# Kernel optimization log

Measured on AMD Instinct MI355X. Metric: run time of the kernel, lower is better.

## Reference

```python
import jax, jax.numpy as jnp
import numpy as np

N_NODES = 100000
N_EDGES = 1600000
IN_CH = 128
HID = 64
OUT_CH = 16
N_GRAPHS = 512
NEG_SLOPE = 0.2


def setup_inputs() -> dict:
    key = jax.random.key(0)
    ks = jax.random.split(key, 24)
    x = jax.random.normal(ks[0], (N_NODES, IN_CH), dtype=jnp.float32)
    edge_index = jax.random.randint(ks[1], (2, N_EDGES), 0, N_NODES, dtype=jnp.int64)
    batch = jnp.sort(jax.random.randint(ks[2], (N_NODES,), 0, N_GRAPHS, dtype=jnp.int64))
    s = 0.05
    p = {
        'W_l1': jax.random.normal(ks[3], (IN_CH, HID)) * s,
        'b_l1': jnp.zeros((HID,), jnp.float32),
        'W_r1': jax.random.normal(ks[4], (IN_CH, HID)) * s,
        'b_r1': jnp.zeros((HID,), jnp.float32),
        'att1': jax.random.normal(ks[5], (HID,)) * s,
        'bias1': jnp.zeros((HID,), jnp.float32),
        'W_l2': jax.random.normal(ks[6], (HID, HID)) * s,
        'b_l2': jnp.zeros((HID,), jnp.float32),
        'W_r2': jax.random.normal(ks[7], (HID, HID)) * s,
        'b_r2': jnp.zeros((HID,), jnp.float32),
        'att2': jax.random.normal(ks[8], (HID,)) * s,
        'bias2': jnp.zeros((HID,), jnp.float32),
        'W_fc1': jax.random.normal(ks[9], (HID, HID)) * s,
        'b_fc1': jnp.zeros((HID,), jnp.float32),
        'gamma': jnp.ones((HID,), jnp.float32),
        'beta': jnp.zeros((HID,), jnp.float32),
        'W_fc2': jax.random.normal(ks[10], (HID, OUT_CH)) * s,
        'b_fc2': jnp.zeros((OUT_CH,), jnp.float32),
    }
    return dict(x=x, edge_index=edge_index, batch=batch, **p)


def _gatv2_layer(x, src, dst, Wl, bl, Wr, br, att, bias):
    # GATv2Conv (heads=1): x_l = lin_l(x), x_r = lin_r(x)
    xl = x @ Wl + bl              # [N, H] source transform
    xr = x @ Wr + br              # [N, H] target transform
    # per-edge score: att . LeakyReLU(x_l[j] + x_r[i])
    h = xl[src] + xr[dst]         # [E, H]
    h = jnp.where(h >= 0, h, NEG_SLOPE * h)
    e = h @ att                   # [E]
    # scatter-softmax over incoming edges of each target node
    m = jax.ops.segment_max(e, dst, num_segments=N_NODES)
    a = jnp.exp(e - m[dst])
    z = jax.ops.segment_sum(a, dst, num_segments=N_NODES)
    alpha = a / z[dst]            # every node has a self-loop -> z > 0
    out = jax.ops.segment_sum(alpha[:, None] * xl[src], dst, num_segments=N_NODES)
    return out + bias


def reference(x, edge_index, batch, W_l1, b_l1, W_r1, b_r1, att1, bias1,
              W_l2, b_l2, W_r2, b_r2, att2, bias2,
              W_fc1, b_fc1, gamma, beta, W_fc2, b_fc2):
    loop = jnp.arange(N_NODES, dtype=edge_index.dtype)
    src = jnp.concatenate([edge_index[0], loop])  # add_self_loops=True
    dst = jnp.concatenate([edge_index[1], loop])
    h = _gatv2_layer(x, src, dst, W_l1, b_l1, W_r1, b_r1, att1, bias1)
    h = jax.nn.relu(h)
    h = _gatv2_layer(h, src, dst, W_l2, b_l2, W_r2, b_r2, att2, bias2)
    # global mean pool over graphs
    sums = jax.ops.segment_sum(h, batch, num_segments=N_GRAPHS)
    cnt = jax.ops.segment_sum(jnp.ones((N_NODES,), h.dtype), batch, num_segments=N_GRAPHS)
    g = sums / jnp.clip(cnt, 1.0)[:, None]        # [G, H]
    # MLP head: Linear -> BatchNorm1d (training-mode batch stats) -> ReLU -> Linear
    y = g @ W_fc1 + b_fc1
    mu = jnp.mean(y, axis=0)
    var = jnp.var(y, axis=0)
    y = gamma * (y - mu) * jax.lax.rsqrt(var + 1e-5) + beta
    y = jax.nn.relu(y)
    y = y @ W_fc2 + b_fc2
    return jax.nn.log_softmax(y, axis=1)
```

## Files before the change

kernel.cpp:

```cpp
#include <hip/hip_runtime.h>

#define N_NODES 100000
#define N_EDGES 1600000
#define IN_CH 128
#define HID 64
#define OUT_CH 16
#define N_GRAPHS 512
#define NEG_SLOPE 0.2f

#define MAX_DEG 64

#define GEMM1_BLOCKS ((N_NODES + 127) / 128)
#define DEG_EPT 8
#define DEG_BLOCKS ((N_EDGES + 256 * DEG_EPT - 1) / (256 * DEG_EPT))
#define FUSED_BLOCKS (GEMM1_BLOCKS + DEG_BLOCKS)

#define NEG_BIG (-1e30f)
#define LDSP 132

__device__ __forceinline__ unsigned int f2bf_pack(float lo, float hi) {
  unsigned int ul = __float_as_uint(lo);
  unsigned int uh = __float_as_uint(hi);
  ul = (ul + 0x7FFFu + ((ul >> 16) & 1u)) >> 16;
  uh = (uh + 0x7FFFu + ((uh >> 16) & 1u)) >> 16;
  return ul | (uh << 16);
}
__device__ __forceinline__ float bf2f(unsigned short b) {
  return __uint_as_float(((unsigned int)b) << 16);
}


__global__ __launch_bounds__(256) void k_fused_gemm1_scatter(
    const float* __restrict__ x,
    const float* __restrict__ Wl, const float* __restrict__ bl,
    const float* __restrict__ Wr, const float* __restrict__ br,
    unsigned short* __restrict__ xlb, unsigned short* __restrict__ xrb,
    const int* __restrict__ src, const int* __restrict__ dst,
    int* __restrict__ deg, int* __restrict__ adjP) {
  constexpr int K = IN_CH;
  constexpr int KC = 16;
  constexpr int NCH = K / KC;
  __shared__ float xs[KC][LDSP];
  __shared__ float ws[KC][LDSP];

  int b = blockIdx.x;
  if (b & 1) {
    int db = b >> 1;
    int base = (db * 256 + threadIdx.x) * DEG_EPT;
    if (base + DEG_EPT <= N_EDGES) {
      int4 d4a = *(const int4*)&dst[base];
      int4 d4b = *(const int4*)&dst[base + 4];
      int4 s4a = *(const int4*)&src[base];
      int4 s4b = *(const int4*)&src[base + 4];
      int sl;
      sl = atomicAdd(&deg[d4a.x], 1); if (sl < MAX_DEG) adjP[d4a.x * MAX_DEG + sl] = s4a.x;
      sl = atomicAdd(&deg[d4a.y], 1); if (sl < MAX_DEG) adjP[d4a.y * MAX_DEG + sl] = s4a.y;
      sl = atomicAdd(&deg[d4a.z], 1); if (sl < MAX_DEG) adjP[d4a.z * MAX_DEG + sl] = s4a.z;
      sl = atomicAdd(&deg[d4a.w], 1); if (sl < MAX_DEG) adjP[d4a.w * MAX_DEG + sl] = s4a.w;
      sl = atomicAdd(&deg[d4b.x], 1); if (sl < MAX_DEG) adjP[d4b.x * MAX_DEG + sl] = s4b.x;
      sl = atomicAdd(&deg[d4b.y], 1); if (sl < MAX_DEG) adjP[d4b.y * MAX_DEG + sl] = s4b.y;
      sl = atomicAdd(&deg[d4b.z], 1); if (sl < MAX_DEG) adjP[d4b.z * MAX_DEG + sl] = s4b.z;
      sl = atomicAdd(&deg[d4b.w], 1); if (sl < MAX_DEG) adjP[d4b.w * MAX_DEG + sl] = s4b.w;
    } else {
      for (int e = base; e < N_EDGES; e++) {
        int d = dst[e];
        int sl = atomicAdd(&deg[d], 1);
        if (sl < MAX_DEG) adjP[d * MAX_DEG + sl] = src[e];
      }
    }
    return;
  }

  int tid = threadIdx.x;
  int tx = tid & 15;
  int ty = tid >> 4;
  int nb = (b >> 1) * 128;

  float acc[8][8];
  #pragma unroll
  for (int i = 0; i < 8; i++)
    #pragma unroll
    for (int j = 0; j < 8; j++) acc[i][j] = 0.f;

  for (int c = 0; c < NCH; c++) {
    int kc = c * KC;
    if (c) __syncthreads();
    #pragma unroll
    for (int j = 0; j < 2; j++) {
      int idx = tid + 256 * j;
      int node = idx >> 2, q = idx & 3;
      int gn = nb + node;
      float4 v = make_float4(0.f, 0.f, 0.f, 0.f);
      if (gn < N_NODES) v = *(const float4*)&x[(size_t)gn * K + kc + q * 4];
      xs[q * 4 + 0][node] = v.x;
      xs[q * 4 + 1][node] = v.y;
      xs[q * 4 + 2][node] = v.z;
      xs[q * 4 + 3][node] = v.w;
    }
    #pragma unroll
    for (int j = 0; j < 2; j++) {
      int idx = tid + 256 * j;
      int k = idx >> 5, cc = idx & 31;
      float4 v;
      if (cc < 16) v = *(const float4*)&Wl[(size_t)(kc + k) * 64 + cc * 4];
      else         v = *(const float4*)&Wr[(size_t)(kc + k) * 64 + (cc - 16) * 4];
      *(float4*)&ws[k][cc * 4] = v;
    }
    __syncthreads();

    #pragma unroll 4
    for (int k = 0; k < KC; k++) {
      float4 a0 = *(const float4*)&xs[k][ty * 8];
      float4 a1 = *(const float4*)&xs[k][ty * 8 + 4];
      float4 b0 = *(const float4*)&ws[k][tx * 8];
      float4 b1 = *(const float4*)&ws[k][tx * 8 + 4];
      float av[8] = {a0.x, a0.y, a0.z, a0.w, a1.x, a1.y, a1.z, a1.w};
      float bv[8] = {b0.x, b0.y, b0.z, b0.w, b1.x, b1.y, b1.z, b1.w};
      #pragma unroll
      for (int i = 0; i < 8; i++)
        #pragma unroll
        for (int j = 0; j < 8; j++)
          acc[i][j] = fmaf(av[i], bv[j], acc[i][j]);
    }
  }

  int f0 = tx * 8;
  float bb[8];
  #pragma unroll
  for (int j = 0; j < 8; j++)
    bb[j] = (f0 < 64) ? bl[f0 + j] : br[f0 - 64 + j];
  unsigned short* outp = (f0 < 64) ? xlb : xrb;
  int fo = (f0 < 64) ? f0 : f0 - 64;
  #pragma unroll
  for (int i = 0; i < 8; i++) {
    int node = nb + ty * 8 + i;
    if (node < N_NODES) {
      int4 o;
      o.x = (int)f2bf_pack(acc[i][0] + bb[0], acc[i][1] + bb[1]);
      o.y = (int)f2bf_pack(acc[i][2] + bb[2], acc[i][3] + bb[3]);
      o.z = (int)f2bf_pack(acc[i][4] + bb[4], acc[i][5] + bb[5]);
      o.w = (int)f2bf_pack(acc[i][6] + bb[6], acc[i][7] + bb[7]);
      *(int4*)&outp[(size_t)node * 64 + fo] = o;
    }
  }
}


template <int K>
__global__ __launch_bounds__(256) void k_dual_gemm(
    const float* __restrict__ x,
    const float* __restrict__ Wl, const float* __restrict__ bl,
    const float* __restrict__ Wr, const float* __restrict__ br,
    unsigned short* __restrict__ xlb, unsigned short* __restrict__ xrb) {
  constexpr int KC = 32;
  constexpr int NCH = K / KC;
  __shared__ float xs[KC][LDSP];
  __shared__ float ws[KC][LDSP];

  int tid = threadIdx.x;
  int tx = tid & 15;
  int ty = tid >> 4;
  int nb = blockIdx.x * 128;

  float acc[8][8];
  #pragma unroll
  for (int i = 0; i < 8; i++)
    #pragma unroll
    for (int j = 0; j < 8; j++) acc[i][j] = 0.f;

  for (int c = 0; c < NCH; c++) {
    int kc = c * KC;
    if (c) __syncthreads();
    #pragma unroll
    for (int j = 0; j < 4; j++) {
      int idx = tid + 256 * j;
      int node = idx >> 3, q = idx & 7;
      int gn = nb + node;
      float4 v = make_float4(0.f, 0.f, 0.f, 0.f);
      if (gn < N_NODES) v = *(const float4*)&x[(size_t)gn * K + kc + q * 4];
      xs[q * 4 + 0][node] = v.x;
      xs[q * 4 + 1][node] = v.y;
      xs[q * 4 + 2][node] = v.z;
      xs[q * 4 + 3][node] = v.w;
    }
    #pragma unroll
    for (int j = 0; j < 4; j++) {
      int idx = tid + 256 * j;
      int k = idx >> 5, cc = idx & 31;
      float4 v;
      if (cc < 16) v = *(const float4*)&Wl[(size_t)(kc + k) * 64 + cc * 4];
      else         v = *(const float4*)&Wr[(size_t)(kc + k) * 64 + (cc - 16) * 4];
      *(float4*)&ws[k][cc * 4] = v;
    }
    __syncthreads();

    #pragma unroll 4
    for (int k = 0; k < KC; k++) {
      float4 a0 = *(const float4*)&xs[k][ty * 8];
      float4 a1 = *(const float4*)&xs[k][ty * 8 + 4];
      float4 b0 = *(const float4*)&ws[k][tx * 8];
      float4 b1 = *(const float4*)&ws[k][tx * 8 + 4];
      float av[8] = {a0.x, a0.y, a0.z, a0.w, a1.x, a1.y, a1.z, a1.w};
      float bv[8] = {b0.x, b0.y, b0.z, b0.w, b1.x, b1.y, b1.z, b1.w};
      #pragma unroll
      for (int i = 0; i < 8; i++)
        #pragma unroll
        for (int j = 0; j < 8; j++)
          acc[i][j] = fmaf(av[i], bv[j], acc[i][j]);
    }
  }

  int f0 = tx * 8;
  float bb[8];
  #pragma unroll
  for (int j = 0; j < 8; j++)
    bb[j] = (f0 < 64) ? bl[f0 + j] : br[f0 - 64 + j];
  unsigned short* outp = (f0 < 64) ? xlb : xrb;
  int fo = (f0 < 64) ? f0 : f0 - 64;
  #pragma unroll
  for (int i = 0; i < 8; i++) {
    int node = nb + ty * 8 + i;
    if (node < N_NODES) {
      int4 o;
      o.x = (int)f2bf_pack(acc[i][0] + bb[0], acc[i][1] + bb[1]);
      o.y = (int)f2bf_pack(acc[i][2] + bb[2], acc[i][3] + bb[3]);
      o.z = (int)f2bf_pack(acc[i][4] + bb[4], acc[i][5] + bb[5]);
      o.w = (int)f2bf_pack(acc[i][6] + bb[6], acc[i][7] + bb[7]);
      *(int4*)&outp[(size_t)node * 64 + fo] = o;
    }
  }
}


__global__ __launch_bounds__(256) void k_gat(
    const unsigned short* __restrict__ xlb, const unsigned short* __restrict__ xrb,
    const float* __restrict__ att, const float* __restrict__ bias,
    const int* __restrict__ deg, const int* __restrict__ adjP,
    float* __restrict__ out, int do_relu) {
  int wid = (blockIdx.x * 256 + threadIdx.x) >> 6;
  int lane = threadIdx.x & 63;
  if (wid >= N_NODES) return;
  int fg = lane & 15;
  int sub = lane >> 4;

  int degv = deg[wid];
  degv = (degv < MAX_DEG) ? degv : MAX_DEG;
  int L = degv + 1;

  int eidx = wid;
  if (lane < degv) eidx = adjP[(size_t)wid * MAX_DEG + lane];

  ushort4 xrr = *(const ushort4*)&xrb[(size_t)wid * 64 + fg * 4];
  float4 xr4;
  xr4.x = bf2f(xrr.x); xr4.y = bf2f(xrr.y); xr4.z = bf2f(xrr.z); xr4.w = bf2f(xrr.w);
  float4 att4 = *(const float4*)&att[fg * 4];

  float m = NEG_BIG, z = 0.f;
  float4 acc = make_float4(0.f, 0.f, 0.f, 0.f);

  for (int p0 = 0; p0 < L; p0 += 8) {
    int q0 = p0 + sub * 2;
    int q1 = q0 + 1;
    bool act0 = (q0 < L);
    bool act1 = (q1 < L);
    int idx0 = q0 - 1;
    int idx1 = q1 - 1;
    int sj0 = __shfl(eidx, idx0 & 63, 64);
    int sj1 = __shfl(eidx, idx1 & 63, 64);
    int j0 = (q0 == 0) ? wid : sj0;
    int j1 = sj1;
    ushort4 raw0 = make_ushort4(0, 0, 0, 0);
    ushort4 raw1 = make_ushort4(0, 0, 0, 0);
    if (act0) raw0 = *(const ushort4*)&xlb[(size_t)j0 * 64 + fg * 4];
    if (act1) raw1 = *(const ushort4*)&xlb[(size_t)j1 * 64 + fg * 4];
    float4 v0, v1;
    v0.x = bf2f(raw0.x); v0.y = bf2f(raw0.y); v0.z = bf2f(raw0.z); v0.w = bf2f(raw0.w);
    v1.x = bf2f(raw1.x); v1.y = bf2f(raw1.y); v1.z = bf2f(raw1.z); v1.w = bf2f(raw1.w);

    float ax, ay, az, aw;
    ax = v0.x + xr4.x; ax = (ax >= 0.f) ? ax : NEG_SLOPE * ax;
    ay = v0.y + xr4.y; ay = (ay >= 0.f) ? ay : NEG_SLOPE * ay;
    az = v0.z + xr4.z; az = (az >= 0.f) ? az : NEG_SLOPE * az;
    aw = v0.w + xr4.w; aw = (aw >= 0.f) ? aw : NEG_SLOPE * aw;
    float s0 = fmaf(ax, att4.x, fmaf(ay, att4.y, fmaf(az, att4.z, aw * att4.w)));
    ax = v1.x + xr4.x; ax = (ax >= 0.f) ? ax : NEG_SLOPE * ax;
    ay = v1.y + xr4.y; ay = (ay >= 0.f) ? ay : NEG_SLOPE * ay;
    az = v1.z + xr4.z; az = (az >= 0.f) ? az : NEG_SLOPE * az;
    aw = v1.w + xr4.w; aw = (aw >= 0.f) ? aw : NEG_SLOPE * aw;
    float s1 = fmaf(ax, att4.x, fmaf(ay, att4.y, fmaf(az, att4.z, aw * att4.w)));
    #pragma unroll
    for (int o = 1; o <= 8; o <<= 1) {
      s0 += __shfl_xor(s0, o, 64);
      s1 += __shfl_xor(s1, o, 64);
    }
    float e0 = act0 ? s0 : NEG_BIG;
    float e1 = act1 ? s1 : NEG_BIG;

    float nm = fmaxf(m, fmaxf(e0, e1));
    float sc = __expf(m - nm);
    float w0 = __expf(e0 - nm);
    float w1 = __expf(e1 - nm);
    z = fmaf(z, sc, w0 + w1);
    acc.x = fmaf(acc.x, sc, fmaf(w0, v0.x, w1 * v1.x));
    acc.y = fmaf(acc.y, sc, fmaf(w0, v0.y, w1 * v1.y));
    acc.z = fmaf(acc.z, sc, fmaf(w0, v0.z, w1 * v1.z));
    acc.w = fmaf(acc.w, sc, fmaf(w0, v0.w, w1 * v1.w));
    m = nm;
  }

  #pragma unroll
  for (int o = 16; o <= 32; o <<= 1) {
    float m2 = __shfl_xor(m, o, 64);
    float z2 = __shfl_xor(z, o, 64);
    float a0 = __shfl_xor(acc.x, o, 64);
    float a1 = __shfl_xor(acc.y, o, 64);
    float a2 = __shfl_xor(acc.z, o, 64);
    float a3 = __shfl_xor(acc.w, o, 64);
    float nm = fmaxf(m, m2);
    float s1 = __expf(m - nm);
    float s2 = __expf(m2 - nm);
    z = z * s1 + z2 * s2;
    acc.x = acc.x * s1 + a0 * s2;
    acc.y = acc.y * s1 + a1 * s2;
    acc.z = acc.z * s1 + a2 * s2;
    acc.w = acc.w * s1 + a3 * s2;
    m = nm;
  }

  if (sub == 0) {
    float4 b4 = *(const float4*)&bias[fg * 4];
    float inv = 1.f / z;
    float4 r;
    r.x = acc.x * inv + b4.x;
    r.y = acc.y * inv + b4.y;
    r.z = acc.z * inv + b4.z;
    r.w = acc.w * inv + b4.w;
    if (do_relu) {
      r.x = fmaxf(r.x, 0.f); r.y = fmaxf(r.y, 0.f);
      r.z = fmaxf(r.z, 0.f); r.w = fmaxf(r.w, 0.f);
    }
    *(float4*)&out[(size_t)wid * 64 + fg * 4] = r;
  }
}


__device__ __forceinline__ int lower_bound_batch(const int* __restrict__ b, int key) {
  int lo = 0, hi = N_NODES;
  while (lo < hi) {
    int mid = (lo + hi) >> 1;
    if (b[mid] < key) lo = mid + 1; else hi = mid;
  }
  return lo;
}

__global__ void k_pool(const float* __restrict__ h, const int* __restrict__ batch,
                       float* __restrict__ gmean) {
  __shared__ int s_range[2];
  __shared__ float red[256];
  int g = blockIdx.x, t = threadIdx.x;
  if (t == 0) s_range[0] = lower_bound_batch(batch, g);
  if (t == 1) s_range[1] = lower_bound_batch(batch, g + 1);
  __syncthreads();
  int lo = s_range[0], hi = s_range[1];
  int f = t & 63, sub = t >> 6;
  float acc = 0.f;
  for (int n = lo + sub; n < hi; n += 4) acc += h[n * 64 + f];
  red[t] = acc;
  __syncthreads();
  if (sub == 0) {
    float s = red[f] + red[64 + f] + red[128 + f] + red[192 + f];
    int cnt = hi - lo;
    if (cnt < 1) cnt = 1;
    gmean[g * 64 + f] = s / (float)cnt;
  }
}


__global__ void k_head1(const float* __restrict__ gmean, const float* __restrict__ W,
                        const float* __restrict__ b, float* __restrict__ y) {
  int idx = blockIdx.x * 256 + threadIdx.x;
  if (idx >= N_GRAPHS * 64) return;
  int gi = idx >> 6, f = idx & 63;
  float acc = b[f];
  #pragma unroll 8
  for (int k = 0; k < 64; k++) acc = fmaf(gmean[gi * 64 + k], W[k * 64 + f], acc);
  y[idx] = acc;
}

__global__ void k_bnstats(const float* __restrict__ y, float* __restrict__ mu,
                          float* __restrict__ rstd) {
  __shared__ float red_s[256], red_ss[256];
  int t = threadIdx.x;
  int f = t & 63, grp = t >> 6;
  float s = 0.f, ss = 0.f;
  for (int g = grp; g < N_GRAPHS; g += 4) {
    float v = y[g * 64 + f];
    s += v;
    ss += v * v;
  }
  red_s[t] = s;
  red_ss[t] = ss;
  __syncthreads();
  if (t < 64) {
    s = red_s[t] + red_s[64 + t] + red_s[128 + t] + red_s[192 + t];
    ss = red_ss[t] + red_ss[64 + t] + red_ss[128 + t] + red_ss[192 + t];
    float m = s / (float)N_GRAPHS;
    float var = ss / (float)N_GRAPHS - m * m;
    mu[t] = m;
    rstd[t] = rsqrtf(var + 1e-5f);
  }
}

__global__ void k_head2(const float* __restrict__ y, const float* __restrict__ gamma,
                        const float* __restrict__ beta, const float* __restrict__ mu,
                        const float* __restrict__ rstd, const float* __restrict__ W2,
                        const float* __restrict__ b2, float* __restrict__ out) {
  int idx = blockIdx.x * 256 + threadIdx.x;
  if (idx >= N_GRAPHS * OUT_CH) return;
  int gi = idx >> 4, o = idx & 15;
  float acc = b2[o];
  #pragma unroll
  for (int k = 0; k < 64; k++) {
    float v = y[gi * 64 + k];
    v = gamma[k] * (v - mu[k]) * rstd[k] + beta[k];
    v = fmaxf(v, 0.f);
    acc = fmaf(v, W2[k * OUT_CH + o], acc);
  }
  float mx = acc;
  #pragma unroll
  for (int w = 8; w > 0; w >>= 1) mx = fmaxf(mx, __shfl_xor(mx, w, 16));
  float ex = __expf(acc - mx);
  float s = ex;
  #pragma unroll
  for (int w = 8; w > 0; w >>= 1) s += __shfl_xor(s, w, 16);
  out[idx] = acc - mx - __logf(s);
}


extern "C" void kernel_launch(void* const* d_in, const int* in_sizes, int n_in,
                              void* d_out, int out_size, void* d_ws, size_t ws_size,
                              hipStream_t stream) {
  const float* x      = (const float*)d_in[0];
  const int*   edge   = (const int*)d_in[1];
  const int*   batch  = (const int*)d_in[2];
  const float* W_l1   = (const float*)d_in[3];
  const float* b_l1   = (const float*)d_in[4];
  const float* W_r1   = (const float*)d_in[5];
  const float* b_r1   = (const float*)d_in[6];
  const float* att1   = (const float*)d_in[7];
  const float* bias1  = (const float*)d_in[8];
  const float* W_l2   = (const float*)d_in[9];
  const float* b_l2   = (const float*)d_in[10];
  const float* W_r2   = (const float*)d_in[11];
  const float* b_r2   = (const float*)d_in[12];
  const float* att2   = (const float*)d_in[13];
  const float* bias2  = (const float*)d_in[14];
  const float* W_fc1  = (const float*)d_in[15];
  const float* b_fc1  = (const float*)d_in[16];
  const float* gamma  = (const float*)d_in[17];
  const float* beta   = (const float*)d_in[18];
  const float* W_fc2  = (const float*)d_in[19];
  const float* b_fc2  = (const float*)d_in[20];

  const int* src = edge;
  const int* dst = edge + N_EDGES;

  char* ws = (char*)d_ws;
  size_t off = 0;
  auto alloc = [&](size_t bytes) -> void* {
    off = (off + 255) & ~(size_t)255;
    void* p = ws + off;
    off += bytes;
    return p;
  };
  int* deg      = (int*)alloc((size_t)N_NODES * 4);
  int* adjP     = (int*)alloc((size_t)N_NODES * MAX_DEG * 4);
  unsigned short* xlb = (unsigned short*)alloc((size_t)N_NODES * HID * 2);
  unsigned short* xrb = (unsigned short*)alloc((size_t)N_NODES * HID * 2);
  float* h      = (float*)alloc((size_t)N_NODES * HID * 4);
  float* gmean  = (float*)alloc((size_t)N_GRAPHS * HID * 4);
  float* y      = (float*)alloc((size_t)N_GRAPHS * HID * 4);
  float* mu     = (float*)alloc(64 * 4);
  float* rstd   = (float*)alloc(64 * 4);

  hipMemsetAsync(deg, 0, (size_t)N_NODES * 4, stream);

  k_fused_gemm1_scatter<<<FUSED_BLOCKS, 256, 0, stream>>>(
      x, W_l1, b_l1, W_r1, b_r1, xlb, xrb, src, dst, deg, adjP);

  k_gat<<<(N_NODES + 3) / 4, 256, 0, stream>>>(xlb, xrb, att1, bias1, deg, adjP, h, 1);
  k_dual_gemm<HID><<<(N_NODES + 127) / 128, 256, 0, stream>>>(h, W_l2, b_l2, W_r2, b_r2, xlb, xrb);
  k_gat<<<(N_NODES + 3) / 4, 256, 0, stream>>>(xlb, xrb, att2, bias2, deg, adjP, h, 0);

  k_pool<<<N_GRAPHS, 256, 0, stream>>>(h, batch, gmean);
  k_head1<<<(N_GRAPHS * 64 + 255) / 256, 256, 0, stream>>>(gmean, W_fc1, b_fc1, y);
  k_bnstats<<<1, 256, 0, stream>>>(y, mu, rstd);
  k_head2<<<(N_GRAPHS * OUT_CH + 255) / 256, 256, 0, stream>>>(y, gamma, beta, mu, rstd,
                                                               W_fc2, b_fc2, (float*)d_out);
}
```

Baseline: 438.8 us.

## Partition edge scatter into destination-range buckets across 8 block groups

```diff
diff --git a/kernel.cpp b/kernel.cpp
--- a/kernel.cpp
+++ b/kernel.cpp
@@ -13,7 +13,9 @@
 #define GEMM1_BLOCKS ((N_NODES + 127) / 128)
 #define DEG_EPT 8
 #define DEG_BLOCKS ((N_EDGES + 256 * DEG_EPT - 1) / (256 * DEG_EPT))
-#define FUSED_BLOCKS (GEMM1_BLOCKS + DEG_BLOCKS)
+#define SCAT_BLOCKS (DEG_BLOCKS * 8)
+#define FUSED_BLOCKS (SCAT_BLOCKS + GEMM1_BLOCKS)
+#define NODES_PER_BUCKET (N_NODES / 8)
 
 #define NEG_BIG (-1e30f)
 #define LDSP 132
@@ -44,28 +46,33 @@
   __shared__ float ws[KC][LDSP];
 
   int b = blockIdx.x;
-  if (b & 1) {
-    int db = b >> 1;
-    int base = (db * 256 + threadIdx.x) * DEG_EPT;
+  if (b < SCAT_BLOCKS) {
+    int w = b >> 3;
+    int myb = b & 7;
+    int lo = myb * NODES_PER_BUCKET;
+    int hi = lo + NODES_PER_BUCKET;
+    int base = (w * 256 + threadIdx.x) * DEG_EPT;
     if (base + DEG_EPT <= N_EDGES) {
       int4 d4a = *(const int4*)&dst[base];
       int4 d4b = *(const int4*)&dst[base + 4];
       int4 s4a = *(const int4*)&src[base];
       int4 s4b = *(const int4*)&src[base + 4];
       int sl;
-      sl = atomicAdd(&deg[d4a.x], 1); if (sl < MAX_DEG) adjP[d4a.x * MAX_DEG + sl] = s4a.x;
-      sl = atomicAdd(&deg[d4a.y], 1); if (sl < MAX_DEG) adjP[d4a.y * MAX_DEG + sl] = s4a.y;
-      sl = atomicAdd(&deg[d4a.z], 1); if (sl < MAX_DEG) adjP[d4a.z * MAX_DEG + sl] = s4a.z;
-      sl = atomicAdd(&deg[d4a.w], 1); if (sl < MAX_DEG) adjP[d4a.w * MAX_DEG + sl] = s4a.w;
-      sl = atomicAdd(&deg[d4b.x], 1); if (sl < MAX_DEG) adjP[d4b.x * MAX_DEG + sl] = s4b.x;
-      sl = atomicAdd(&deg[d4b.y], 1); if (sl < MAX_DEG) adjP[d4b.y * MAX_DEG + sl] = s4b.y;
-      sl = atomicAdd(&deg[d4b.z], 1); if (sl < MAX_DEG) adjP[d4b.z * MAX_DEG + sl] = s4b.z;
-      sl = atomicAdd(&deg[d4b.w], 1); if (sl < MAX_DEG) adjP[d4b.w * MAX_DEG + sl] = s4b.w;
+      if (d4a.x >= lo && d4a.x < hi) { sl = atomicAdd(&deg[d4a.x], 1); if (sl < MAX_DEG) adjP[d4a.x * MAX_DEG + sl] = s4a.x; }
+      if (d4a.y >= lo && d4a.y < hi) { sl = atomicAdd(&deg[d4a.y], 1); if (sl < MAX_DEG) adjP[d4a.y * MAX_DEG + sl] = s4a.y; }
+      if (d4a.z >= lo && d4a.z < hi) { sl = atomicAdd(&deg[d4a.z], 1); if (sl < MAX_DEG) adjP[d4a.z * MAX_DEG + sl] = s4a.z; }
+      if (d4a.w >= lo && d4a.w < hi) { sl = atomicAdd(&deg[d4a.w], 1); if (sl < MAX_DEG) adjP[d4a.w * MAX_DEG + sl] = s4a.w; }
+      if (d4b.x >= lo && d4b.x < hi) { sl = atomicAdd(&deg[d4b.x], 1); if (sl < MAX_DEG) adjP[d4b.x * MAX_DEG + sl] = s4b.x; }
+      if (d4b.y >= lo && d4b.y < hi) { sl = atomicAdd(&deg[d4b.y], 1); if (sl < MAX_DEG) adjP[d4b.y * MAX_DEG + sl] = s4b.y; }
+      if (d4b.z >= lo && d4b.z < hi) { sl = atomicAdd(&deg[d4b.z], 1); if (sl < MAX_DEG) adjP[d4b.z * MAX_DEG + sl] = s4b.z; }
+      if (d4b.w >= lo && d4b.w < hi) { sl = atomicAdd(&deg[d4b.w], 1); if (sl < MAX_DEG) adjP[d4b.w * MAX_DEG + sl] = s4b.w; }
     } else {
       for (int e = base; e < N_EDGES; e++) {
         int d = dst[e];
-        int sl = atomicAdd(&deg[d], 1);
-        if (sl < MAX_DEG) adjP[d * MAX_DEG + sl] = src[e];
+        if (d >= lo && d < hi) {
+          int sl = atomicAdd(&deg[d], 1);
+          if (sl < MAX_DEG) adjP[d * MAX_DEG + sl] = src[e];
+        }
       }
     }
     return;
@@ -74,7 +81,7 @@
   int tid = threadIdx.x;
   int tx = tid & 15;
   int ty = tid >> 4;
-  int nb = (b >> 1) * 128;
+  int nb = (b - SCAT_BLOCKS) * 128;
 
   float acc[8][8];
   #pragma unroll
```

After: 462.2 us. 5.3% more time.

## Build adjacency via bucketed counting sort instead of global atomics

Applied to the files above, without the earlier changes.

```diff
diff --git a/kernel.cpp b/kernel.cpp
--- a/kernel.cpp
+++ b/kernel.cpp
@@ -10,10 +10,9 @@
 
 #define MAX_DEG 64
 
-#define GEMM1_BLOCKS ((N_NODES + 127) / 128)
-#define DEG_EPT 8
-#define DEG_BLOCKS ((N_EDGES + 256 * DEG_EPT - 1) / (256 * DEG_EPT))
-#define FUSED_BLOCKS (GEMM1_BLOCKS + DEG_BLOCKS)
+#define NBUCK ((N_NODES + 255) >> 8)
+#define NCB 128
+#define EDGE_WIN ((N_EDGES + NCB - 1) / NCB)
 
 #define NEG_BIG (-1e30f)
 #define LDSP 132
@@ -30,119 +29,91 @@
 }
 
 
-__global__ __launch_bounds__(256) void k_fused_gemm1_scatter(
-    const float* __restrict__ x,
-    const float* __restrict__ Wl, const float* __restrict__ bl,
-    const float* __restrict__ Wr, const float* __restrict__ br,
-    unsigned short* __restrict__ xlb, unsigned short* __restrict__ xrb,
-    const int* __restrict__ src, const int* __restrict__ dst,
-    int* __restrict__ deg, int* __restrict__ adjP) {
-  constexpr int K = IN_CH;
-  constexpr int KC = 16;
-  constexpr int NCH = K / KC;
-  __shared__ float xs[KC][LDSP];
-  __shared__ float ws[KC][LDSP];
-
-  int b = blockIdx.x;
-  if (b & 1) {
-    int db = b >> 1;
-    int base = (db * 256 + threadIdx.x) * DEG_EPT;
-    if (base + DEG_EPT <= N_EDGES) {
-      int4 d4a = *(const int4*)&dst[base];
-      int4 d4b = *(const int4*)&dst[base + 4];
-      int4 s4a = *(const int4*)&src[base];
-      int4 s4b = *(const int4*)&src[base + 4];
-      int sl;
-      sl = atomicAdd(&deg[d4a.x], 1); if (sl < MAX_DEG) adjP[d4a.x * MAX_DEG + sl] = s4a.x;
-      sl = atomicAdd(&deg[d4a.y], 1); if (sl < MAX_DEG) adjP[d4a.y * MAX_DEG + sl] = s4a.y;
-      sl = atomicAdd(&deg[d4a.z], 1); if (sl < MAX_DEG) adjP[d4a.z * MAX_DEG + sl] = s4a.z;
-      sl = atomicAdd(&deg[d4a.w], 1); if (sl < MAX_DEG) adjP[d4a.w * MAX_DEG + sl] = s4a.w;
-      sl = atomicAdd(&deg[d4b.x], 1); if (sl < MAX_DEG) adjP[d4b.x * MAX_DEG + sl] = s4b.x;
-      sl = atomicAdd(&deg[d4b.y], 1); if (sl < MAX_DEG) adjP[d4b.y * MAX_DEG + sl] = s4b.y;
-      sl = atomicAdd(&deg[d4b.z], 1); if (sl < MAX_DEG) adjP[d4b.z * MAX_DEG + sl] = s4b.z;
-      sl = atomicAdd(&deg[d4b.w], 1); if (sl < MAX_DEG) adjP[d4b.w * MAX_DEG + sl] = s4b.w;
-    } else {
-      for (int e = base; e < N_EDGES; e++) {
-        int d = dst[e];
-        int sl = atomicAdd(&deg[d], 1);
-        if (sl < MAX_DEG) adjP[d * MAX_DEG + sl] = src[e];
-      }
-    }
-    return;
-  }
-
-  int tid = threadIdx.x;
-  int tx = tid & 15;
-  int ty = tid >> 4;
-  int nb = (b >> 1) * 128;
-
-  float acc[8][8];
-  #pragma unroll
-  for (int i = 0; i < 8; i++)
-    #pragma unroll
-    for (int j = 0; j < 8; j++) acc[i][j] = 0.f;
-
-  for (int c = 0; c < NCH; c++) {
-    int kc = c * KC;
-    if (c) __syncthreads();
-    #pragma unroll
-    for (int j = 0; j < 2; j++) {
-      int idx = tid + 256 * j;
-      int node = idx >> 2, q = idx & 3;
-      int gn = nb + node;
-      float4 v = make_float4(0.f, 0.f, 0.f, 0.f);
-      if (gn < N_NODES) v = *(const float4*)&x[(size_t)gn * K + kc + q * 4];
-      xs[q * 4 + 0][node] = v.x;
-      xs[q * 4 + 1][node] = v.y;
-      xs[q * 4 + 2][node] = v.z;
-      xs[q * 4 + 3][node] = v.w;
-    }
-    #pragma unroll
-    for (int j = 0; j < 2; j++) {
-      int idx = tid + 256 * j;
-      int k = idx >> 5, cc = idx & 31;
-      float4 v;
-      if (cc < 16) v = *(const float4*)&Wl[(size_t)(kc + k) * 64 + cc * 4];
-      else         v = *(const float4*)&Wr[(size_t)(kc + k) * 64 + (cc - 16) * 4];
-      *(float4*)&ws[k][cc * 4] = v;
-    }
+__global__ __launch_bounds__(256) void k_count(const int* __restrict__ dst,
+                                               int* __restrict__ hist) {
+  __shared__ int hloc[NBUCK];
+  int b = blockIdx.x, t = threadIdx.x;
+  for (int j = t; j < NBUCK; j += 256) hloc[j] = 0;
+  __syncthreads();
+  int lo = b * EDGE_WIN;
+  int hi = lo + EDGE_WIN;
+  if (hi > N_EDGES) hi = N_EDGES;
+  for (int e = lo + t; e < hi; e += 256)
+    atomicAdd(&hloc[dst[e] >> 8], 1);
+  __syncthreads();
+  for (int j = t; j < NBUCK; j += 256) hist[j * NCB + b] = hloc[j];
+}
+
+
+__global__ __launch_bounds__(512) void k_scan(int* __restrict__ hist,
+                                              int* __restrict__ base) {
+  __shared__ int tot[512];
+  int t = threadIdx.x;
+  int total = 0;
+  if (t < NBUCK) {
+    int run = 0;
+    for (int b = 0; b < NCB; b++) {
+      int v = hist[t * NCB + b];
+      hist[t * NCB + b] = run;
+      run += v;
+    }
+    total = run;
+  }
+  tot[t] = total;
+  __syncthreads();
+  for (int o = 1; o < 512; o <<= 1) {
+    int v = (t >= o) ? tot[t - o] : 0;
     __syncthreads();
-
-    #pragma unroll 4
-    for (int k = 0; k < KC; k++) {
-      float4 a0 = *(const float4*)&xs[k][ty * 8];
-      float4 a1 = *(const float4*)&xs[k][ty * 8 + 4];
-      float4 b0 = *(const float4*)&ws[k][tx * 8];
-      float4 b1 = *(const float4*)&ws[k][tx * 8 + 4];
-      float av[8] = {a0.x, a0.y, a0.z, a0.w, a1.x, a1.y, a1.z, a1.w};
-      float bv[8] = {b0.x, b0.y, b0.z, b0.w, b1.x, b1.y, b1.z, b1.w};
-      #pragma unroll
-      for (int i = 0; i < 8; i++)
-        #pragma unroll
-        for (int j = 0; j < 8; j++)
-          acc[i][j] = fmaf(av[i], bv[j], acc[i][j]);
-    }
-  }
-
-  int f0 = tx * 8;
-  float bb[8];
-  #pragma unroll
-  for (int j = 0; j < 8; j++)
-    bb[j] = (f0 < 64) ? bl[f0 + j] : br[f0 - 64 + j];
-  unsigned short* outp = (f0 < 64) ? xlb : xrb;
-  int fo = (f0 < 64) ? f0 : f0 - 64;
-  #pragma unroll
-  for (int i = 0; i < 8; i++) {
-    int node = nb + ty * 8 + i;
-    if (node < N_NODES) {
-      int4 o;
-      o.x = (int)f2bf_pack(acc[i][0] + bb[0], acc[i][1] + bb[1]);
-      o.y = (int)f2bf_pack(acc[i][2] + bb[2], acc[i][3] + bb[3]);
-      o.z = (int)f2bf_pack(acc[i][4] + bb[4], acc[i][5] + bb[5]);
-      o.w = (int)f2bf_pack(acc[i][6] + bb[6], acc[i][7] + bb[7]);
-      *(int4*)&outp[(size_t)node * 64 + fo] = o;
-    }
-  }
+    tot[t] += v;
+    __syncthreads();
+  }
+  int excl = (t == 0) ? 0 : tot[t - 1];
+  if (t < NBUCK) {
+    base[t] = excl;
+    for (int b = 0; b < NCB; b++) hist[t * NCB + b] += excl;
+  }
+  if (t == NBUCK) base[NBUCK] = excl;
+}
+
+
+__global__ __launch_bounds__(256) void k_scatter(const int* __restrict__ src,
+                                                 const int* __restrict__ dst,
+                                                 const int* __restrict__ hist,
+                                                 int* __restrict__ eS, int* __restrict__ eD) {
+  __shared__ int cur[NBUCK];
+  int b = blockIdx.x, t = threadIdx.x;
+  for (int j = t; j < NBUCK; j += 256) cur[j] = hist[j * NCB + b];
+  __syncthreads();
+  int lo = b * EDGE_WIN;
+  int hi = lo + EDGE_WIN;
+  if (hi > N_EDGES) hi = N_EDGES;
+  for (int e = lo + t; e < hi; e += 256) {
+    int d = dst[e];
+    int pos = atomicAdd(&cur[d >> 8], 1);
+    eD[pos] = d;
+    eS[pos] = src[e];
+  }
+}
+
+
+__global__ __launch_bounds__(256) void k_build(const int* __restrict__ eS,
+                                               const int* __restrict__ eD,
+                                               const int* __restrict__ base,
+                                               int* __restrict__ deg, int* __restrict__ adjP) {
+  __shared__ int cnt[256];
+  int j = blockIdx.x, t = threadIdx.x;
+  cnt[t] = 0;
+  __syncthreads();
+  int lo = base[j], hi = base[j + 1];
+  int nb = j << 8;
+  for (int e = lo + t; e < hi; e += 256) {
+    int d = eD[e], s = eS[e];
+    int sl = atomicAdd(&cnt[d - nb], 1);
+    if (sl < MAX_DEG) adjP[d * MAX_DEG + sl] = s;
+  }
+  __syncthreads();
+  int n = nb + t;
+  if (n < N_NODES) deg[n] = cnt[t];
 }
 
 
@@ -482,11 +453,18 @@
   float* y      = (float*)alloc((size_t)N_GRAPHS * HID * 4);
   float* mu     = (float*)alloc(64 * 4);
   float* rstd   = (float*)alloc(64 * 4);
-
-  hipMemsetAsync(deg, 0, (size_t)N_NODES * 4, stream);
-
-  k_fused_gemm1_scatter<<<FUSED_BLOCKS, 256, 0, stream>>>(
-      x, W_l1, b_l1, W_r1, b_r1, xlb, xrb, src, dst, deg, adjP);
+  int* hist     = (int*)alloc((size_t)NBUCK * NCB * 4);
+  int* base     = (int*)alloc((size_t)(NBUCK + 1) * 4);
+
+  int* eS = (int*)h;
+  int* eD = eS + N_EDGES;
+
+  k_count<<<NCB, 256, 0, stream>>>(dst, hist);
+  k_scan<<<1, 512, 0, stream>>>(hist, base);
+  k_scatter<<<NCB, 256, 0, stream>>>(src, dst, hist, eS, eD);
+  k_build<<<NBUCK, 256, 0, stream>>>(eS, eD, base, deg, adjP);
+
+  k_dual_gemm<IN_CH><<<(N_NODES + 127) / 128, 256, 0, stream>>>(x, W_l1, b_l1, W_r1, b_r1, xlb, xrb);
 
   k_gat<<<(N_NODES + 3) / 4, 256, 0, stream>>>(xlb, xrb, att1, bias1, deg, adjP, h, 1);
   k_dual_gemm<HID><<<(N_NODES + 127) / 128, 256, 0, stream>>>(h, W_l2, b_l2, W_r2, b_r2, xlb, xrb);
```

New measurement: 493.1 us. 1.12x slower.
